# Kernel tuning notes

Measured on AMD Instinct MI355X. Metric: run time of the kernel, lower is better.

The kernel has to match this reference:

```python
import jax, jax.numpy as jnp
import numpy as np

R, S, D_IN, WIDTH, K = 8192, 128, 16, 64, 8  # rays, samples/ray, feat dim, net_width, net_kernels


def setup_inputs() -> dict:
    key = jax.random.key(0)
    ks = jax.random.split(key, 8)
    he = jax.nn.initializers.he_uniform()
    idxs = jax.random.randint(ks[0], (R, S), 0, K, dtype=jnp.int32)
    xs = jax.random.normal(ks[1], (R, S, D_IN), dtype=jnp.float32)
    # MultiMLP params: net_depth=2 hidden MultiDense layers + 1 output layer, each with K kernels
    W0 = he(ks[2], (K, D_IN, WIDTH), jnp.float32)
    b0 = jnp.zeros((K, WIDTH), jnp.float32)
    W1 = he(ks[3], (K, WIDTH, WIDTH), jnp.float32)
    b1 = jnp.zeros((K, WIDTH), jnp.float32)
    W2 = he(ks[4], (K, WIDTH, 1), jnp.float32)
    b2 = jnp.zeros((K, 1), jnp.float32)
    return {"idxs": idxs, "xs": xs, "W0": W0, "b0": b0, "W1": W1, "b1": b1, "W2": W2, "b2": b2}


def _multi_dense(idx, x, W, b):
    """Per-sample kernel select: out[n] = x[n] @ W[idx[n]] + b[idx[n]].

    x: [N, d], W: [K, d, f], b: [K, f], idx: [N] int. Loop is over the small
    fixed kernel count K (not a data dim); avoids materializing an [N, d, f]
    gathered-weight tensor.
    """
    out = jnp.zeros((x.shape[0], W.shape[-1]), x.dtype)
    zero = jnp.zeros((), x.dtype)
    for k in range(W.shape[0]):
        sel = (idx == k)[:, None]
        out = out + jnp.where(sel, x @ W[k] + b[k], zero)
    return out


def reference(idxs, xs, W0, b0, W1, b1, W2, b2):
    batch_shape = idxs.shape  # (R, S)
    idx = idxs.reshape(-1)
    h = xs.reshape(-1, xs.shape[-1])
    h = jax.nn.relu(_multi_dense(idx, h, W0, b0))
    h = jax.nn.relu(_multi_dense(idx, h, W1, b1))
    out = _multi_dense(idx, h, W2, b2)  # [N, 1] density
    return out.reshape(*batch_shape, 1)
```

## Files before the change

### kernel.cpp

```cpp
#include <hip/hip_runtime.h>


typedef __attribute__((ext_vector_type(8))) short bfrag;
typedef __attribute__((ext_vector_type(4))) float ffrag;

#define SPAN        512
#define NSPANS      2048
#define IMG_STRIDE  15360
#define WS_NEED     ((size_t)(8 * IMG_STRIDE))

__device__ __forceinline__ unsigned short bf16r(float f) {
    unsigned int u = __float_as_uint(f);
    u += 0x7fffu + ((u >> 16) & 1u);
    return (unsigned short)(u >> 16);
}
__device__ __forceinline__ unsigned int pack_trunc(float hiF, float loF) {
    return __builtin_amdgcn_perm(__float_as_uint(hiF), __float_as_uint(loF), 0x07060302u);
}
__device__ __forceinline__ unsigned int pack_rnd(float hiF, float loF) {
    return __builtin_amdgcn_perm(__float_as_uint(hiF) + 0x8000u,
                                 __float_as_uint(loF) + 0x8000u, 0x07060302u);
}

__global__ void k_build_images(const float* __restrict__ W0, const float* __restrict__ b0,
                               const float* __restrict__ W1, const float* __restrict__ b1,
                               const float* __restrict__ W2, const float* __restrict__ b2,
                               unsigned char* __restrict__ wsB) {
    const int k = blockIdx.x, t = threadIdx.x;
    unsigned char* img = wsB + k * IMG_STRIDE;
    unsigned short* w0b = (unsigned short*)img;
    unsigned short* w1b = (unsigned short*)(img + 4096);
    unsigned short* w2b = (unsigned short*)(img + 12288);
    float* bias = (float*)(img + 14336);
    for (int e = t; e < 2048; e += 256) {
        int j = e & 7, lane = (e >> 3) & 63, nt = e >> 9, q = lane >> 4;
        int kk = q * 8 + j;
        w0b[e] = (kk < 16) ? bf16r(W0[k * 1024 + kk * 64 + nt * 16 + (lane & 15)])
                           : (unsigned short)0;
    }
    for (int e = t; e < 4096; e += 256) {
        int j = e & 7, lane = (e >> 3) & 63, s = (e >> 9) & 1, nt = e >> 10, q = lane >> 4;
        int h = (j & 3) * 16 + s * 8 + q * 2 + (j >> 2);
        w1b[e] = bf16r(W1[k * 4096 + h * 64 + nt * 16 + (lane & 15)]);
    }
    for (int e = t; e < 1024; e += 256) {
        int j = e & 7, lane = (e >> 3) & 63, s = e >> 9, q = lane >> 4, l15 = lane & 15;
        int h = (j & 3) * 16 + s * 8 + q * 2 + (j >> 2);
        w2b[e] = (l15 == 0) ? bf16r(W2[k * 64 + h]) : (unsigned short)0;
    }
    if (t < 64) bias[t] = b0[k * 64 + t];
    else if (t < 128) bias[t] = b1[k * 64 + (t - 64)];
    else if (t == 128) bias[128] = b2[k];
}

__global__ __launch_bounds__(256, 4) void k_fused(const int* __restrict__ idxs,
                                                  const float* __restrict__ xs,
                                                  const unsigned char* __restrict__ wsB,
                                                  float* __restrict__ out) {
    __shared__ int wcnt[2][4][8];
    __shared__ int bsbase[2][4][8];
    __shared__ int cntS[8], startS[8];
    __shared__ unsigned short sId[SPAN];
    __shared__ __align__(16) unsigned short Xg[SPAN * 16];
    __shared__ __align__(16) unsigned short H3[4][16 * 72];
    __shared__ float outBuf[SPAN];

    const int tid = threadIdx.x, lane = tid & 63, w = tid >> 6;
    const int q = lane >> 4, l15 = lane & 15;
    const int base = blockIdx.x * SPAN;

    int kreg[2], lrank[2];
    #pragma unroll
    for (int it = 0; it < 2; ++it) {
        int k = idxs[base + it * 256 + tid];
        kreg[it] = k;
        unsigned long long mymask = 0;
        #pragma unroll
        for (int kk = 0; kk < 8; ++kk) {
            unsigned long long m = __ballot(k == kk);
            if (k == kk) mymask = m;
            if (lane == 0) wcnt[it][w][kk] = (int)__popcll(m);
        }
        lrank[it] = (int)__popcll(mymask & ((1ull << lane) - 1ull));
    }
    __syncthreads();
    if (tid < 8) {
        int c = 0;
        for (int it = 0; it < 2; ++it)
            for (int w2 = 0; w2 < 4; ++w2) c += wcnt[it][w2][tid];
        cntS[tid] = c;
    }
    __syncthreads();
    if (tid == 0) {
        int s = 0;
        for (int k = 0; k < 8; ++k) { startS[k] = s; s += cntS[k]; }
    }
    __syncthreads();
    if (tid < 64) {
        int it = tid >> 5, w2 = (tid >> 3) & 3, kk = tid & 7;
        int b = startS[kk];
        for (int it2 = 0; it2 < it; ++it2)
            for (int w3 = 0; w3 < 4; ++w3) b += wcnt[it2][w3][kk];
        for (int w3 = 0; w3 < w2; ++w3) b += wcnt[it][w3][kk];
        bsbase[it][w2][kk] = b;
    }
    __syncthreads();
    #pragma unroll
    for (int it = 0; it < 2; ++it)
        sId[bsbase[it][w][kreg[it]] + lrank[it]] = (unsigned short)(it * 256 + tid);
    __syncthreads();

    #pragma unroll
    for (int it = 0; it < 2; ++it) {
        const int r = it * 256 + tid;
        const int gid = base + (int)sId[r];
        const float4* p = (const float4*)(xs + (size_t)gid * 16);
        float4 f0 = p[0], f1 = p[1], f2 = p[2], f3 = p[3];
        uint4 lo, hi;
        lo.x = pack_trunc(f0.y, f0.x); lo.y = pack_trunc(f0.w, f0.z);
        lo.z = pack_trunc(f1.y, f1.x); lo.w = pack_trunc(f1.w, f1.z);
        hi.x = pack_trunc(f2.y, f2.x); hi.y = pack_trunc(f2.w, f2.z);
        hi.z = pack_trunc(f3.y, f3.x); hi.w = pack_trunc(f3.w, f3.z);
        const int g = r >> 4, m = r & 15;
        *(uint4*)(Xg + g * 256 + m * 8)       = lo;
        *(uint4*)(Xg + g * 256 + 128 + m * 8) = hi;
    }
    __syncthreads();

    unsigned short* H = H3[w];
    #pragma unroll
    for (int kk2 = 0; kk2 < 2; ++kk2) {
        const int k = w + kk2 * 4;
        const int cnt = cntS[k];
        if (cnt == 0) continue;
        const int start = startS[k];
        const unsigned char* img = wsB + k * IMG_STRIDE;

        bfrag w0f[4], w1f[4][2], w2f[2];
        #pragma unroll
        for (int nt = 0; nt < 4; ++nt)
            w0f[nt] = *(const bfrag*)(img + nt * 1024 + lane * 16);
        #pragma unroll
        for (int nt = 0; nt < 4; ++nt)
            #pragma unroll
            for (int s = 0; s < 2; ++s)
                w1f[nt][s] = *(const bfrag*)(img + 4096 + ((nt * 2 + s) * 64 + lane) * 16);
        #pragma unroll
        for (int s = 0; s < 2; ++s)
            w2f[s] = *(const bfrag*)(img + 12288 + (s * 64 + lane) * 16);
        const float* bias = (const float*)(img + 14336);
        float b0v[4], b1v[4];
        #pragma unroll
        for (int nt = 0; nt < 4; ++nt) {
            b0v[nt] = bias[nt * 16 + l15];
            b1v[nt] = bias[64 + nt * 16 + l15];
        }
        const float b2v = bias[128];

        const int nst = (cnt + 15) >> 4;

        auto loadA = [&](int st) -> bfrag {
            int R = start + st * 16 + l15;
            int Rm = start + cnt - 1;
            R = R < Rm ? R : Rm;
            bfrag av = {0, 0, 0, 0, 0, 0, 0, 0};
            if (q < 2)
                av = *(const bfrag*)(Xg + (R >> 4) * 256 + q * 128 + (R & 15) * 8);
            return av;
        };

        bfrag aCur = loadA(0);
        for (int st = 0; st < nst; ++st) {
            ffrag acc0[4];
            #pragma unroll
            for (int nt = 0; nt < 4; ++nt) {
                ffrag z = {0.f, 0.f, 0.f, 0.f};
                acc0[nt] = __builtin_amdgcn_mfma_f32_16x16x32_bf16(aCur, w0f[nt], z, 0, 0, 0);
            }
            bfrag aNxt = {0, 0, 0, 0, 0, 0, 0, 0};
            if (st + 1 < nst) aNxt = loadA(st + 1);

            #pragma unroll
            for (int r = 0; r < 4; ++r) {
                float v0 = acc0[0][r] + b0v[0]; v0 = v0 > 0.f ? v0 : 0.f;
                float v1 = acc0[1][r] + b0v[1]; v1 = v1 > 0.f ? v1 : 0.f;
                float v2 = acc0[2][r] + b0v[2]; v2 = v2 > 0.f ? v2 : 0.f;
                float v3 = acc0[3][r] + b0v[3]; v3 = v3 > 0.f ? v3 : 0.f;
                uint2 u;
                u.x = pack_rnd(v1, v0);
                u.y = pack_rnd(v3, v2);
                *(uint2*)((unsigned char*)H + (q * 4 + r) * 144 + l15 * 8) = u;
            }

            bfrag a10 = *(const bfrag*)((unsigned char*)H + l15 * 144 + q * 16);
            bfrag a11 = *(const bfrag*)((unsigned char*)H + l15 * 144 + 64 + q * 16);
            ffrag acc1[4];
            #pragma unroll
            for (int nt = 0; nt < 4; ++nt) {
                ffrag z = {0.f, 0.f, 0.f, 0.f};
                acc1[nt] = __builtin_amdgcn_mfma_f32_16x16x32_bf16(a10, w1f[nt][0], z, 0, 0, 0);
                acc1[nt] = __builtin_amdgcn_mfma_f32_16x16x32_bf16(a11, w1f[nt][1], acc1[nt], 0, 0, 0);
            }

            #pragma unroll
            for (int r = 0; r < 4; ++r) {
                float v0 = acc1[0][r] + b1v[0]; v0 = v0 > 0.f ? v0 : 0.f;
                float v1 = acc1[1][r] + b1v[1]; v1 = v1 > 0.f ? v1 : 0.f;
                float v2 = acc1[2][r] + b1v[2]; v2 = v2 > 0.f ? v2 : 0.f;
                float v3 = acc1[3][r] + b1v[3]; v3 = v3 > 0.f ? v3 : 0.f;
                uint2 u;
                u.x = pack_rnd(v1, v0);
                u.y = pack_rnd(v3, v2);
                *(uint2*)((unsigned char*)H + (q * 4 + r) * 144 + l15 * 8) = u;
            }

            bfrag a20 = *(const bfrag*)((unsigned char*)H + l15 * 144 + q * 16);
            bfrag a21 = *(const bfrag*)((unsigned char*)H + l15 * 144 + 64 + q * 16);
            ffrag d;
            {
                ffrag z = {0.f, 0.f, 0.f, 0.f};
                d = __builtin_amdgcn_mfma_f32_16x16x32_bf16(a20, w2f[0], z, 0, 0, 0);
                d = __builtin_amdgcn_mfma_f32_16x16x32_bf16(a21, w2f[1], d, 0, 0, 0);
            }

            if (l15 == 0) {
                #pragma unroll
                for (int r = 0; r < 4; ++r) {
                    int row = st * 16 + q * 4 + r;
                    if (row < cnt) {
                        int oid = (int)sId[start + row];
                        outBuf[oid] = d[r] + b2v;
                    }
                }
            }

            aCur = aNxt;
        }
    }
    __syncthreads();

    ((float2*)(out + base))[tid] = ((const float2*)outBuf)[tid];
}

__global__ void k_fallback(const int* __restrict__ idxs, const float* __restrict__ xs,
                           const float* __restrict__ W0, const float* __restrict__ b0,
                           const float* __restrict__ W1, const float* __restrict__ b1,
                           const float* __restrict__ W2, const float* __restrict__ b2,
                           float* __restrict__ out, int N) {
    int n = blockIdx.x * blockDim.x + threadIdx.x;
    if (n >= N) return;
    int k = idxs[n];
    float h0[64];
    #pragma unroll
    for (int j = 0; j < 64; ++j) h0[j] = b0[k * 64 + j];
    for (int i = 0; i < 16; ++i) {
        float xi = xs[(size_t)n * 16 + i];
        #pragma unroll
        for (int j = 0; j < 64; ++j) h0[j] = fmaf(xi, W0[k * 1024 + i * 64 + j], h0[j]);
    }
    #pragma unroll
    for (int j = 0; j < 64; ++j) h0[j] = fmaxf(h0[j], 0.f);
    float acc = b2[k];
    for (int jc = 0; jc < 4; ++jc) {
        float h1[16];
        #pragma unroll
        for (int j = 0; j < 16; ++j) h1[j] = b1[k * 64 + jc * 16 + j];
        for (int i = 0; i < 64; ++i) {
            float hv = h0[i];
            #pragma unroll
            for (int j = 0; j < 16; ++j)
                h1[j] = fmaf(hv, W1[k * 4096 + i * 64 + jc * 16 + j], h1[j]);
        }
        #pragma unroll
        for (int j = 0; j < 16; ++j) acc = fmaf(fmaxf(h1[j], 0.f), W2[k * 64 + jc * 16 + j], acc);
    }
    out[n] = acc;
}

extern "C" void kernel_launch(void* const* d_in, const int* in_sizes, int n_in,
                              void* d_out, int out_size, void* d_ws, size_t ws_size,
                              hipStream_t stream) {
    const int*   idxs = (const int*)d_in[0];
    const float* xs   = (const float*)d_in[1];
    const float* W0   = (const float*)d_in[2];
    const float* b0   = (const float*)d_in[3];
    const float* W1   = (const float*)d_in[4];
    const float* b1   = (const float*)d_in[5];
    const float* W2   = (const float*)d_in[6];
    const float* b2   = (const float*)d_in[7];
    float* out = (float*)d_out;
    const int N = in_sizes[0];

    if (N != SPAN * NSPANS || ws_size < WS_NEED) {
        k_fallback<<<(N + 255) / 256, 256, 0, stream>>>(idxs, xs, W0, b0, W1, b1, W2, b2, out, N);
        return;
    }

    unsigned char* wsB = (unsigned char*)d_ws;
    k_build_images<<<8, 256, 0, stream>>>(W0, b0, W1, b1, W2, b2, wsB);
    k_fused<<<NSPANS, 256, 0, stream>>>(idxs, xs, wsB, out);
}
```

Before: 137.8 us.

## Fold layer-0 bias into MFMA, replace output MFMA with shuffle reduction, prefetch xs unsorted

Layer-0 bias is now folded into the first MFMA by adding a constant-one input column and a matching bias row in the weight image. The final 64->1 layer drops its two MFMAs and the LDS round-trip, using an FMA dot product in fp32 followed by a cross-lane shuffle reduction. xs is loaded in natural order before the sort and written to LDS without gathering, so global loads overlap the ballot/scan phase and one barrier goes away; rows are then looked up through sId when loading A fragments. bf16 packing switches to the library round-to-nearest conversion, which may cost more ALU than the old add-and-permute.

```diff
diff --git a/kernel.cpp b/kernel.cpp
--- a/kernel.cpp
+++ b/kernel.cpp
@@ -1,4 +1,5 @@
 #include <hip/hip_runtime.h>
+#include <hip/hip_bf16.h>
 
 
 typedef __attribute__((ext_vector_type(8))) short bfrag;
@@ -6,7 +7,7 @@
 
 #define SPAN        512
 #define NSPANS      2048
-#define IMG_STRIDE  15360
+#define IMG_STRIDE  13312
 #define WS_NEED     ((size_t)(8 * IMG_STRIDE))
 
 __device__ __forceinline__ unsigned short bf16r(float f) {
@@ -17,9 +18,10 @@
 __device__ __forceinline__ unsigned int pack_trunc(float hiF, float loF) {
     return __builtin_amdgcn_perm(__float_as_uint(hiF), __float_as_uint(loF), 0x07060302u);
 }
-__device__ __forceinline__ unsigned int pack_rnd(float hiF, float loF) {
-    return __builtin_amdgcn_perm(__float_as_uint(hiF) + 0x8000u,
-                                 __float_as_uint(loF) + 0x8000u, 0x07060302u);
+__device__ __forceinline__ unsigned int pack_cvt(float loF, float hiF) {
+    union { __hip_bfloat162 h2; unsigned int u; } c;
+    c.h2 = __float22bfloat162_rn(make_float2(loF, hiF));
+    return c.u;
 }
 
 __global__ void k_build_images(const float* __restrict__ W0, const float* __restrict__ b0,
@@ -30,26 +32,22 @@
     unsigned char* img = wsB + k * IMG_STRIDE;
     unsigned short* w0b = (unsigned short*)img;
     unsigned short* w1b = (unsigned short*)(img + 4096);
-    unsigned short* w2b = (unsigned short*)(img + 12288);
-    float* bias = (float*)(img + 14336);
+    float* bias = (float*)(img + 12288);
     for (int e = t; e < 2048; e += 256) {
         int j = e & 7, lane = (e >> 3) & 63, nt = e >> 9, q = lane >> 4;
-        int kk = q * 8 + j;
-        w0b[e] = (kk < 16) ? bf16r(W0[k * 1024 + kk * 64 + nt * 16 + (lane & 15)])
-                           : (unsigned short)0;
+        int kk = q * 8 + j, n = nt * 16 + (lane & 15);
+        unsigned short v = 0;
+        if (kk < 16) v = bf16r(W0[k * 1024 + kk * 64 + n]);
+        else if (kk == 16) v = bf16r(b0[k * 64 + n]);
+        w0b[e] = v;
     }
     for (int e = t; e < 4096; e += 256) {
         int j = e & 7, lane = (e >> 3) & 63, s = (e >> 9) & 1, nt = e >> 10, q = lane >> 4;
         int h = (j & 3) * 16 + s * 8 + q * 2 + (j >> 2);
         w1b[e] = bf16r(W1[k * 4096 + h * 64 + nt * 16 + (lane & 15)]);
     }
-    for (int e = t; e < 1024; e += 256) {
-        int j = e & 7, lane = (e >> 3) & 63, s = e >> 9, q = lane >> 4, l15 = lane & 15;
-        int h = (j & 3) * 16 + s * 8 + q * 2 + (j >> 2);
-        w2b[e] = (l15 == 0) ? bf16r(W2[k * 64 + h]) : (unsigned short)0;
-    }
-    if (t < 64) bias[t] = b0[k * 64 + t];
-    else if (t < 128) bias[t] = b1[k * 64 + (t - 64)];
+    if (t < 64) bias[t] = b1[k * 64 + t];
+    else if (t < 128) bias[t] = W2[k * 64 + (t - 64)];
     else if (t == 128) bias[128] = b2[k];
 }
 
@@ -69,6 +67,11 @@
     const int q = lane >> 4, l15 = lane & 15;
     const int base = blockIdx.x * SPAN;
 
+    const float4* xp0 = (const float4*)(xs + (size_t)(base + tid) * 16);
+    const float4* xp1 = (const float4*)(xs + (size_t)(base + 256 + tid) * 16);
+    float4 g0 = xp0[0], g1 = xp0[1], g2 = xp0[2], g3 = xp0[3];
+    float4 g4 = xp1[0], g5 = xp1[1], g6 = xp1[2], g7 = xp1[3];
+
     int kreg[2], lrank[2];
     #pragma unroll
     for (int it = 0; it < 2; ++it) {
@@ -108,22 +111,21 @@
     #pragma unroll
     for (int it = 0; it < 2; ++it)
         sId[bsbase[it][w][kreg[it]] + lrank[it]] = (unsigned short)(it * 256 + tid);
-    __syncthreads();
-
-    #pragma unroll
-    for (int it = 0; it < 2; ++it) {
-        const int r = it * 256 + tid;
-        const int gid = base + (int)sId[r];
-        const float4* p = (const float4*)(xs + (size_t)gid * 16);
-        float4 f0 = p[0], f1 = p[1], f2 = p[2], f3 = p[3];
+
+    {
         uint4 lo, hi;
-        lo.x = pack_trunc(f0.y, f0.x); lo.y = pack_trunc(f0.w, f0.z);
-        lo.z = pack_trunc(f1.y, f1.x); lo.w = pack_trunc(f1.w, f1.z);
-        hi.x = pack_trunc(f2.y, f2.x); hi.y = pack_trunc(f2.w, f2.z);
-        hi.z = pack_trunc(f3.y, f3.x); hi.w = pack_trunc(f3.w, f3.z);
-        const int g = r >> 4, m = r & 15;
-        *(uint4*)(Xg + g * 256 + m * 8)       = lo;
-        *(uint4*)(Xg + g * 256 + 128 + m * 8) = hi;
+        lo.x = pack_trunc(g0.y, g0.x); lo.y = pack_trunc(g0.w, g0.z);
+        lo.z = pack_trunc(g1.y, g1.x); lo.w = pack_trunc(g1.w, g1.z);
+        hi.x = pack_trunc(g2.y, g2.x); hi.y = pack_trunc(g2.w, g2.z);
+        hi.z = pack_trunc(g3.y, g3.x); hi.w = pack_trunc(g3.w, g3.z);
+        *(uint4*)(Xg + tid * 16) = lo;
+        *(uint4*)(Xg + tid * 16 + 8) = hi;
+        lo.x = pack_trunc(g4.y, g4.x); lo.y = pack_trunc(g4.w, g4.z);
+        lo.z = pack_trunc(g5.y, g5.x); lo.w = pack_trunc(g5.w, g5.z);
+        hi.x = pack_trunc(g6.y, g6.x); hi.y = pack_trunc(g6.w, g6.z);
+        hi.z = pack_trunc(g7.y, g7.x); hi.w = pack_trunc(g7.w, g7.z);
+        *(uint4*)(Xg + (256 + tid) * 16) = lo;
+        *(uint4*)(Xg + (256 + tid) * 16 + 8) = hi;
     }
     __syncthreads();
 
@@ -136,7 +138,7 @@
         const int start = startS[k];
         const unsigned char* img = wsB + k * IMG_STRIDE;
 
-        bfrag w0f[4], w1f[4][2], w2f[2];
+        bfrag w0f[4], w1f[4][2];
         #pragma unroll
         for (int nt = 0; nt < 4; ++nt)
             w0f[nt] = *(const bfrag*)(img + nt * 1024 + lane * 16);
@@ -145,31 +147,35 @@
             #pragma unroll
             for (int s = 0; s < 2; ++s)
                 w1f[nt][s] = *(const bfrag*)(img + 4096 + ((nt * 2 + s) * 64 + lane) * 16);
-        #pragma unroll
-        for (int s = 0; s < 2; ++s)
-            w2f[s] = *(const bfrag*)(img + 12288 + (s * 64 + lane) * 16);
-        const float* bias = (const float*)(img + 14336);
-        float b0v[4], b1v[4];
+        const float* bias = (const float*)(img + 12288);
+        float b1v[4], w2v[4];
         #pragma unroll
         for (int nt = 0; nt < 4; ++nt) {
-            b0v[nt] = bias[nt * 16 + l15];
-            b1v[nt] = bias[64 + nt * 16 + l15];
+            b1v[nt] = bias[nt * 16 + l15];
+            w2v[nt] = bias[64 + nt * 16 + l15];
         }
         const float b2v = bias[128];
 
         const int nst = (cnt + 15) >> 4;
 
-        auto loadA = [&](int st) -> bfrag {
+        auto loadA = [&](int st, bfrag* a, int* rowid) {
             int R = start + st * 16 + l15;
             int Rm = start + cnt - 1;
             R = R < Rm ? R : Rm;
+            int row = (int)sId[R];
+            *rowid = row;
             bfrag av = {0, 0, 0, 0, 0, 0, 0, 0};
             if (q < 2)
-                av = *(const bfrag*)(Xg + (R >> 4) * 256 + q * 128 + (R & 15) * 8);
-            return av;
+                av = *(const bfrag*)(Xg + row * 16 + q * 8);
+            else if (q == 2)
+                av[0] = (short)0x3F80;
+            *a = av;
         };
 
-        bfrag aCur = loadA(0);
+        bfrag aCur;
+        int rowCur;
+        loadA(0, &aCur, &rowCur);
+
         for (int st = 0; st < nst; ++st) {
             ffrag acc0[4];
             #pragma unroll
@@ -178,17 +184,18 @@
                 acc0[nt] = __builtin_amdgcn_mfma_f32_16x16x32_bf16(aCur, w0f[nt], z, 0, 0, 0);
             }
             bfrag aNxt = {0, 0, 0, 0, 0, 0, 0, 0};
-            if (st + 1 < nst) aNxt = loadA(st + 1);
+            int rowNxt = 0;
+            if (st + 1 < nst) loadA(st + 1, &aNxt, &rowNxt);
 
             #pragma unroll
             for (int r = 0; r < 4; ++r) {
-                float v0 = acc0[0][r] + b0v[0]; v0 = v0 > 0.f ? v0 : 0.f;
-                float v1 = acc0[1][r] + b0v[1]; v1 = v1 > 0.f ? v1 : 0.f;
-                float v2 = acc0[2][r] + b0v[2]; v2 = v2 > 0.f ? v2 : 0.f;
-                float v3 = acc0[3][r] + b0v[3]; v3 = v3 > 0.f ? v3 : 0.f;
+                float v0 = acc0[0][r]; v0 = v0 > 0.f ? v0 : 0.f;
+                float v1 = acc0[1][r]; v1 = v1 > 0.f ? v1 : 0.f;
+                float v2 = acc0[2][r]; v2 = v2 > 0.f ? v2 : 0.f;
+                float v3 = acc0[3][r]; v3 = v3 > 0.f ? v3 : 0.f;
                 uint2 u;
-                u.x = pack_rnd(v1, v0);
-                u.y = pack_rnd(v3, v2);
+                u.x = pack_cvt(v0, v1);
+                u.y = pack_cvt(v2, v3);
                 *(uint2*)((unsigned char*)H + (q * 4 + r) * 144 + l15 * 8) = u;
             }
 
@@ -204,37 +211,23 @@
 
             #pragma unroll
             for (int r = 0; r < 4; ++r) {
-                float v0 = acc1[0][r] + b1v[0]; v0 = v0 > 0.f ? v0 : 0.f;
-                float v1 = acc1[1][r] + b1v[1]; v1 = v1 > 0.f ? v1 : 0.f;
-                float v2 = acc1[2][r] + b1v[2]; v2 = v2 > 0.f ? v2 : 0.f;
-                float v3 = acc1[3][r] + b1v[3]; v3 = v3 > 0.f ? v3 : 0.f;
-                uint2 u;
-                u.x = pack_rnd(v1, v0);
-                u.y = pack_rnd(v3, v2);
-                *(uint2*)((unsigned char*)H + (q * 4 + r) * 144 + l15 * 8) = u;
-            }
-
-            bfrag a20 = *(const bfrag*)((unsigned char*)H + l15 * 144 + q * 16);
-            bfrag a21 = *(const bfrag*)((unsigned char*)H + l15 * 144 + 64 + q * 16);
-            ffrag d;
-            {
-                ffrag z = {0.f, 0.f, 0.f, 0.f};
-                d = __builtin_amdgcn_mfma_f32_16x16x32_bf16(a20, w2f[0], z, 0, 0, 0);
-                d = __builtin_amdgcn_mfma_f32_16x16x32_bf16(a21, w2f[1], d, 0, 0, 0);
-            }
-
-            if (l15 == 0) {
+                float p = 0.f;
                 #pragma unroll
-                for (int r = 0; r < 4; ++r) {
-                    int row = st * 16 + q * 4 + r;
-                    if (row < cnt) {
-                        int oid = (int)sId[start + row];
-                        outBuf[oid] = d[r] + b2v;
-                    }
+                for (int nt = 0; nt < 4; ++nt) {
+                    float h = acc1[nt][r] + b1v[nt];
+                    h = h > 0.f ? h : 0.f;
+                    p = fmaf(h, w2v[nt], p);
                 }
+                p += __shfl_xor(p, 1);
+                p += __shfl_xor(p, 2);
+                p += __shfl_xor(p, 4);
+                p += __shfl_xor(p, 8);
+                if (l15 == q * 4 + r && st * 16 + l15 < cnt)
+                    outBuf[rowCur] = p + b2v;
             }
 
             aCur = aNxt;
+            rowCur = rowNxt;
         }
     }
     __syncthreads();
```

Result: slower. 143.7 us (+4.3%).
